# Kernel optimization log

Hardware: AMD Instinct MI355X
Metric: run time of the kernel (lower is better)

The kernel has to match this reference:

```python
import jax, jax.numpy as jnp
import numpy as np

D_MODEL = 1024
N_HEADS = 16
D_K = D_MODEL // N_HEADS


def setup_inputs() -> dict:
    key = jax.random.key(0)
    ks = jax.random.split(key, 9)
    B, S, D = 2, 2048, D_MODEL
    q = jax.random.normal(ks[0], (B, S, D), dtype=jnp.float32)
    v = jax.random.normal(ks[1], (B, S, D), dtype=jnp.float32)
    k = jax.random.normal(ks[2], (B, S, D), dtype=jnp.float32)
    att_mask = jnp.zeros((B, S, S), dtype=jnp.float32)
    seq_mask = jax.random.uniform(ks[3], (B, S, S), dtype=jnp.float32)
    scale = 1.0 / np.sqrt(D)
    Wq = jax.random.normal(ks[4], (D, D), dtype=jnp.float32) * scale
    Wk = jax.random.normal(ks[5], (D, D), dtype=jnp.float32) * scale
    Wv = jax.random.normal(ks[6], (D, D), dtype=jnp.float32) * scale
    Wo = jax.random.normal(ks[7], (D, D), dtype=jnp.float32) * scale
    return {"q": q, "v": v, "k": k, "att_mask": att_mask, "seq_mask": seq_mask,
            "Wq": Wq, "Wk": Wk, "Wv": Wv, "Wo": Wo}


def _split_heads(x, B):
    # [B, S, D] -> [B, H, S, d_k]
    return x.reshape(B, -1, N_HEADS, D_K).transpose(0, 2, 1, 3)


def reference(q, v, k, att_mask, seq_mask, Wq, Wk, Wv, Wo):
    B = q.shape[0]
    qh = _split_heads(q @ Wq, B)
    kh = _split_heads(k @ Wk, B)
    vh = _split_heads(v @ Wv, B)
    # scores: [B, H, Sq, Sk]
    scores = jnp.einsum('bhqd,bhkd->bhqk', qh, kh) / jnp.sqrt(jnp.float32(D_K))
    scores = scores + att_mask[:, None]
    attn = jax.nn.softmax(scores, axis=-1)
    attn = attn * seq_mask[:, None]  # post-softmax multiplicative mask
    out = jnp.einsum('bhqk,bhkd->bhqd', attn, vh)
    out = out.transpose(0, 2, 1, 3).reshape(B, -1, D_MODEL)
    return out @ Wo
```

## Files before the change

kernel.cpp:

```cpp
#include <hip/hip_runtime.h>
#include <cstddef>

typedef __attribute__((ext_vector_type(8))) short s16x8;
typedef __attribute__((ext_vector_type(4))) float f32x4;
typedef __attribute__((ext_vector_type(4))) unsigned short us4;

static __device__ __forceinline__ float bf2f(unsigned short u) {
    union { unsigned u; float f; } v;
    v.u = ((unsigned)u) << 16;
    return v.f;
}

static __device__ __forceinline__ unsigned short f2bf(float f) {
    union { float f; unsigned u; } v;
    v.f = f;
    unsigned r = v.u + 0x7fffu + ((v.u >> 16) & 1u);
    return (unsigned short)(r >> 16);
}

static __device__ __forceinline__ unsigned short f2bf_fast(float f) {
    unsigned r;
    asm("v_cvt_pk_bf16_f32 %0, %1, %2" : "=v"(r) : "v"(f), "v"(f));
    return (unsigned short)r;
}

#if __has_builtin(__builtin_amdgcn_exp2f)
#define EXP2F(x) __builtin_amdgcn_exp2f(x)
#else
#define EXP2F(x) exp2f(x)
#endif

static __device__ __forceinline__ float ldf(const unsigned short* p, size_t i) { return bf2f(p[i]); }
static __device__ __forceinline__ float ldf(const float* p, size_t i) { return p[i]; }
static __device__ __forceinline__ void stf(unsigned short* p, size_t i, float v) { p[i] = f2bf(v); }
static __device__ __forceinline__ void stf(float* p, size_t i, float v) { p[i] = v; }

__global__ __launch_bounds__(256) void probe_dtype(
    const unsigned short* __restrict__ q, unsigned* __restrict__ flags)
{
    __shared__ float red[256];
    const int t = threadIdx.x;
    float m = 0.0f;
    for (int i = t; i < 16384; i += 256) {
        float x = fabsf(bf2f(q[i]));
        if (!(x == x)) x = 1.0e30f;
        m = fmaxf(m, x);
    }
    red[t] = m;
    __syncthreads();
    for (int s = 128; s > 0; s >>= 1) {
        if (t < s) red[t] = fmaxf(red[t], red[t + s]);
        __syncthreads();
    }
    if (t == 0) {
        flags[0] = (red[0] < 1000.0f) ? 0u : 1u;
        flags[1] = 0u;
    }
}

__global__ __launch_bounds__(256) void probe_zero(
    const uint4* __restrict__ m, unsigned* __restrict__ flags)
{
    const unsigned dt = flags[0];
    const size_t n = dt ? 2097152u : 1048576u;
    unsigned acc = 0;
    for (size_t i = (size_t)blockIdx.x * 256 + threadIdx.x; i < n;
         i += (size_t)gridDim.x * 256) {
        uint4 v = m[i];
        acc |= v.x | v.y | v.z | v.w;
    }
    if (acc) atomicOr(&flags[1], 1u);
}

__global__ __launch_bounds__(256) void cvt3_f32_bf16(
    const float4* __restrict__ s0, us4* __restrict__ d0,
    const float4* __restrict__ s1, us4* __restrict__ d1,
    const float4* __restrict__ s2, us4* __restrict__ d2,
    unsigned n4, const unsigned* __restrict__ flags)
{
    if (flags[0] != 1u) return;
    const float4* s = (blockIdx.y == 0) ? s0 : (blockIdx.y == 1) ? s1 : s2;
    us4* d = (blockIdx.y == 0) ? d0 : (blockIdx.y == 1) ? d1 : d2;
    for (unsigned i = blockIdx.x * 256u + threadIdx.x; i < n4;
         i += gridDim.x * 256u) {
        float4 v = s[i];
        us4 o;
        o.x = f2bf(v.x); o.y = f2bf(v.y); o.z = f2bf(v.z); o.w = f2bf(v.w);
        d[i] = o;
    }
}

__global__ __launch_bounds__(256) void copy3_bf16(
    const uint4* __restrict__ s0, uint4* __restrict__ d0,
    const uint4* __restrict__ s1, uint4* __restrict__ d1,
    const uint4* __restrict__ s2, uint4* __restrict__ d2,
    unsigned n16, const unsigned* __restrict__ flags)
{
    if (flags[0] != 0u) return;
    const uint4* s = (blockIdx.y == 0) ? s0 : (blockIdx.y == 1) ? s1 : s2;
    uint4* d = (blockIdx.y == 0) ? d0 : (blockIdx.y == 1) ? d1 : d2;
    for (unsigned i = blockIdx.x * 256u + threadIdx.x; i < n16;
         i += gridDim.x * 256u)
        d[i] = s[i];
}

__global__ __launch_bounds__(256) void cvt_f32_bf16(
    const float4* __restrict__ src, us4* __restrict__ dst, unsigned n4,
    const unsigned* __restrict__ flags)
{
    if (flags[0] != 1u) return;
    for (unsigned i = blockIdx.x * 256u + threadIdx.x; i < n4;
         i += gridDim.x * 256u) {
        float4 v = src[i];
        us4 o;
        o.x = f2bf(v.x); o.y = f2bf(v.y); o.z = f2bf(v.z); o.w = f2bf(v.w);
        dst[i] = o;
    }
}

template <typename T>
__global__ __launch_bounds__(256) void transpose_w(
    const T* __restrict__ src, unsigned short* __restrict__ dst,
    const unsigned* __restrict__ flag, unsigned want)
{
    if (*flag != want) return;
    __shared__ unsigned short tile[32][33];
    const int c0 = blockIdx.x * 32, r0 = blockIdx.y * 32;
    const int tx = threadIdx.x, ty = threadIdx.y;
#pragma unroll
    for (int i = 0; i < 32; i += 8)
        tile[ty + i][tx] = f2bf(ldf(src, (size_t)(r0 + ty + i) * 1024 + c0 + tx));
    __syncthreads();
#pragma unroll
    for (int i = 0; i < 32; i += 8)
        dst[(size_t)(c0 + ty + i) * 1024 + r0 + tx] = tile[tx][ty + i];
}

template <typename T>
__global__ __launch_bounds__(256) void transpose_w3(
    const T* __restrict__ s0, const T* __restrict__ s1, const T* __restrict__ s2,
    unsigned short* __restrict__ d0, unsigned short* __restrict__ d1,
    unsigned short* __restrict__ d2,
    const unsigned* __restrict__ flag, unsigned want)
{
    if (*flag != want) return;
    const T* src = (blockIdx.z == 0) ? s0 : (blockIdx.z == 1) ? s1 : s2;
    unsigned short* dst = (blockIdx.z == 0) ? d0 : (blockIdx.z == 1) ? d1 : d2;
    __shared__ unsigned short tile[32][33];
    const int c0 = blockIdx.x * 32, r0 = blockIdx.y * 32;
    const int tx = threadIdx.x, ty = threadIdx.y;
#pragma unroll
    for (int i = 0; i < 32; i += 8)
        tile[ty + i][tx] = f2bf(ldf(src, (size_t)(r0 + ty + i) * 1024 + c0 + tx));
    __syncthreads();
#pragma unroll
    for (int i = 0; i < 32; i += 8)
        dst[(size_t)(c0 + ty + i) * 1024 + r0 + tx] = tile[tx][ty + i];
}

template <typename TO>
__global__ __launch_bounds__(256) void gemm_kernel(
    const unsigned short* __restrict__ A, const unsigned short* __restrict__ Bt,
    TO* __restrict__ out, int mode, const unsigned* __restrict__ flags, unsigned want)
{
    if (want != 2u && flags[0] != want) return;
    const int K = 1024;
    __shared__ __align__(16) unsigned short lA[64 * 72];
    __shared__ __align__(16) unsigned short lB[64 * 72];

    const int m0 = blockIdx.y * 64, n0 = blockIdx.x * 64;
    const int t = threadIdx.x;
    const int w = t >> 6, l = t & 63, quad = l >> 4, l15 = l & 15;
    const int srow = t >> 2, scol = (t & 3) * 16;

    const unsigned short* Arow = A + (size_t)(m0 + srow) * K + scol;
    const unsigned short* Brow = Bt + (size_t)(n0 + srow) * K + scol;

    f32x4 acc[4] = {};

    uint4 a0 = *(const uint4*)(Arow);
    uint4 a1 = *(const uint4*)(Arow + 8);
    uint4 b0 = *(const uint4*)(Brow);
    uint4 b1 = *(const uint4*)(Brow + 8);

    for (int k0 = 0; k0 < K; k0 += 64) {
        *(uint4*)&lA[srow * 72 + scol] = a0;
        *(uint4*)&lA[srow * 72 + scol + 8] = a1;
        *(uint4*)&lB[srow * 72 + scol] = b0;
        *(uint4*)&lB[srow * 72 + scol + 8] = b1;
        __syncthreads();
        const int kn = (k0 + 64) & (K - 1);
        a0 = *(const uint4*)(Arow + kn);
        a1 = *(const uint4*)(Arow + kn + 8);
        b0 = *(const uint4*)(Brow + kn);
        b1 = *(const uint4*)(Brow + kn + 8);
#pragma unroll
        for (int kk = 0; kk < 64; kk += 32) {
            s16x8 af = *(const s16x8*)&lA[(w * 16 + l15) * 72 + kk + quad * 8];
#pragma unroll
            for (int g = 0; g < 4; g++) {
                s16x8 bf = *(const s16x8*)&lB[(g * 16 + l15) * 72 + kk + quad * 8];
                acc[g] = __builtin_amdgcn_mfma_f32_16x16x32_bf16(af, bf, acc[g], 0, 0, 0);
            }
        }
        __syncthreads();
    }

#pragma unroll
    for (int g = 0; g < 4; g++) {
#pragma unroll
        for (int r = 0; r < 4; r++) {
            int row = m0 + w * 16 + quad * 4 + r;
            int col = n0 + g * 16 + l15;
            float val = acc[g][r];
            if (mode == 0) {
                stf(out, (size_t)row * 1024 + col, val);
            } else {
                int b = row >> 11, s = row & 2047;
                int h = col >> 6, d = col & 63;
                if (mode == 1)
                    stf(out, (((size_t)(b * 16 + h) * 2048) + s) * 64 + d, val);
                else
                    stf(out, (((size_t)(b * 16 + h) * 64) + d) * 2048 + s, val);
            }
        }
    }
}

template <typename TM>
__global__ __launch_bounds__(256) void attn_kernel(
    const unsigned short* __restrict__ qh, const unsigned short* __restrict__ kh,
    const unsigned short* __restrict__ vt, const TM* __restrict__ amask,
    const unsigned short* __restrict__ smask, unsigned short* __restrict__ aout,
    const unsigned* __restrict__ flags, unsigned want)
{
    if (flags[0] != want) return;
    const bool useA = (flags[1] != 0u);
    const int S = 2048, DK = 64, H = 16;
    const int qt = blockIdx.x, h = blockIdx.y, b = blockIdx.z;
    const unsigned short* qhb = qh + (size_t)(b * H + h) * S * DK;
    const unsigned short* khb = kh + (size_t)(b * H + h) * S * DK;
    const unsigned short* vtb = vt + (size_t)(b * H + h) * DK * S;
    const TM* amb = amask + (size_t)b * S * S;
    const unsigned short* smb = smask + (size_t)b * S * S;

    __shared__ __align__(16) unsigned short lK[64 * 72];
    __shared__ __align__(16) unsigned short lV[64 * 72];
    __shared__ __align__(16) unsigned short lP[4][16 * 72];

    const int t = threadIdx.x;
    const int w = t >> 6, l = t & 63, quad = l >> 4, l15 = l & 15;
    const int q0 = qt * 64;
    const int srow = t >> 2, scol = (t & 3) * 16;

    const float SCALE2 = 0.18033688011112042f;
    const float LOG2E  = 1.4426950408889634f;

    const int qrow_a = q0 + w * 16 + l15;
    s16x8 qf0 = *(const s16x8*)&qhb[(size_t)qrow_a * DK + quad * 8];
    s16x8 qf1 = *(const s16x8*)&qhb[(size_t)qrow_a * DK + 32 + quad * 8];

    float mrun[4], lsum[4];
    f32x4 o[4] = {};
#pragma unroll
    for (int r = 0; r < 4; r++) { mrun[r] = -INFINITY; lsum[r] = 0.0f; }

    for (int k0 = 0; k0 < S; k0 += 64) {
        const uint4* gk = (const uint4*)&khb[(size_t)(k0 + srow) * DK + scol];
        const uint4* gv = (const uint4*)&vtb[(size_t)srow * S + k0 + scol];
        uint4 ka = gk[0], kb = gk[1];
        uint4 va = gv[0], vb = gv[1];
        *(uint4*)&lK[srow * 72 + scol] = ka;
        *(uint4*)&lK[srow * 72 + scol + 8] = kb;
        *(uint4*)&lV[srow * 72 + scol] = va;
        *(uint4*)&lV[srow * 72 + scol + 8] = vb;
        __syncthreads();

        f32x4 sc[4] = {};
#pragma unroll
        for (int kk = 0; kk < 64; kk += 32) {
            s16x8 af = (kk == 0) ? qf0 : qf1;
#pragma unroll
            for (int g = 0; g < 4; g++) {
                s16x8 bf = *(const s16x8*)&lK[(g * 16 + l15) * 72 + kk + quad * 8];
                sc[g] = __builtin_amdgcn_mfma_f32_16x16x32_bf16(af, bf, sc[g], 0, 0, 0);
            }
        }

        if (!useA) {
#pragma unroll
            for (int r = 0; r < 4; r++) {
                const int qr = q0 + w * 16 + quad * 4 + r;
                const size_t mrow = (size_t)qr * S + k0;
                float sv0 = sc[0][r] * SCALE2;
                float sv1 = sc[1][r] * SCALE2;
                float sv2 = sc[2][r] * SCALE2;
                float sv3 = sc[3][r] * SCALE2;
                float mx = fmaxf(fmaxf(sv0, sv1), fmaxf(sv2, sv3));
#pragma unroll
                for (int d = 1; d < 16; d <<= 1) mx = fmaxf(mx, __shfl_xor(mx, d));
                float mnew = fmaxf(mrun[r], mx);
                float alpha = EXP2F(mrun[r] - mnew);
                float e0 = EXP2F(sv0 - mnew);
                float e1 = EXP2F(sv1 - mnew);
                float e2 = EXP2F(sv2 - mnew);
                float e3 = EXP2F(sv3 - mnew);
                lsum[r] = lsum[r] * alpha + ((e0 + e1) + (e2 + e3));
                mrun[r] = mnew;
#pragma unroll
                for (int g = 0; g < 4; g++) o[g][r] *= alpha;
                const int rowp = (quad * 4 + r) * 72;
                lP[w][rowp + 0 * 16 + l15] = f2bf_fast(e0 * bf2f(smb[mrow + 0 * 16 + l15]));
                lP[w][rowp + 1 * 16 + l15] = f2bf_fast(e1 * bf2f(smb[mrow + 1 * 16 + l15]));
                lP[w][rowp + 2 * 16 + l15] = f2bf_fast(e2 * bf2f(smb[mrow + 2 * 16 + l15]));
                lP[w][rowp + 3 * 16 + l15] = f2bf_fast(e3 * bf2f(smb[mrow + 3 * 16 + l15]));
            }
        } else {
#pragma unroll
            for (int r = 0; r < 4; r++) {
                const int qr = q0 + w * 16 + quad * 4 + r;
                const size_t mrow = (size_t)qr * S + k0;
                float sv0 = fmaf((float)ldf(amb, mrow + 0 * 16 + l15), LOG2E, sc[0][r] * SCALE2);
                float sv1 = fmaf((float)ldf(amb, mrow + 1 * 16 + l15), LOG2E, sc[1][r] * SCALE2);
                float sv2 = fmaf((float)ldf(amb, mrow + 2 * 16 + l15), LOG2E, sc[2][r] * SCALE2);
                float sv3 = fmaf((float)ldf(amb, mrow + 3 * 16 + l15), LOG2E, sc[3][r] * SCALE2);
                float mx = fmaxf(fmaxf(sv0, sv1), fmaxf(sv2, sv3));
#pragma unroll
                for (int d = 1; d < 16; d <<= 1) mx = fmaxf(mx, __shfl_xor(mx, d));
                float mnew = fmaxf(mrun[r], mx);
                float alpha = EXP2F(mrun[r] - mnew);
                float e0 = EXP2F(sv0 - mnew);
                float e1 = EXP2F(sv1 - mnew);
                float e2 = EXP2F(sv2 - mnew);
                float e3 = EXP2F(sv3 - mnew);
                lsum[r] = lsum[r] * alpha + ((e0 + e1) + (e2 + e3));
                mrun[r] = mnew;
#pragma unroll
                for (int g = 0; g < 4; g++) o[g][r] *= alpha;
                const int rowp = (quad * 4 + r) * 72;
                lP[w][rowp + 0 * 16 + l15] = f2bf_fast(e0 * bf2f(smb[mrow + 0 * 16 + l15]));
                lP[w][rowp + 1 * 16 + l15] = f2bf_fast(e1 * bf2f(smb[mrow + 1 * 16 + l15]));
                lP[w][rowp + 2 * 16 + l15] = f2bf_fast(e2 * bf2f(smb[mrow + 2 * 16 + l15]));
                lP[w][rowp + 3 * 16 + l15] = f2bf_fast(e3 * bf2f(smb[mrow + 3 * 16 + l15]));
            }
        }
        __syncthreads();

#pragma unroll
        for (int kk = 0; kk < 64; kk += 32) {
            s16x8 pf = *(const s16x8*)&lP[w][l15 * 72 + kk + quad * 8];
#pragma unroll
            for (int g = 0; g < 4; g++) {
                s16x8 vf = *(const s16x8*)&lV[(g * 16 + l15) * 72 + kk + quad * 8];
                o[g] = __builtin_amdgcn_mfma_f32_16x16x32_bf16(pf, vf, o[g], 0, 0, 0);
            }
        }
        __syncthreads();
    }

#pragma unroll
    for (int r = 0; r < 4; r++) {
        float ls = lsum[r];
#pragma unroll
        for (int d = 1; d < 16; d <<= 1) ls += __shfl_xor(ls, d);
        float inv = 1.0f / ls;
        const int qr = q0 + w * 16 + quad * 4 + r;
#pragma unroll
        for (int g = 0; g < 4; g++) {
            aout[((size_t)(b * S + qr)) * 1024 + h * 64 + g * 16 + l15] =
                f2bf_fast(o[g][r] * inv);
        }
    }
}

extern "C" void kernel_launch(void* const* d_in, const int* in_sizes, int n_in,
                              void* d_out, int out_size, void* d_ws, size_t ws_size,
                              hipStream_t stream)
{
    const void* q   = d_in[0];
    const void* v   = d_in[1];
    const void* k   = d_in[2];
    const void* att = d_in[3];
    const void* seq = d_in[4];
    const void* Wq  = d_in[5];
    const void* Wk  = d_in[6];
    const void* Wv  = d_in[7];
    const void* Wo  = d_in[8];

    const size_t WELEM = 1024 * 1024;
    const size_t HELEM = (size_t)2 * 16 * 2048 * 64;

    unsigned* flags = (unsigned*)d_ws;
    unsigned short* base = (unsigned short*)((char*)d_ws + 512);
    unsigned short* r0 = base;
    unsigned short* qh = base + HELEM;
    unsigned short* kh = qh + HELEM;
    unsigned short* vt = kh + HELEM;
    unsigned short* qb = vt + HELEM;
    unsigned short* kb = qb + HELEM;
    unsigned short* vb = kb + HELEM;
    unsigned short* seqb = qb;

    const dim3 tg(32, 32), tb(32, 8);
    const dim3 tg3(32, 32, 3);
    const dim3 gg(16, 64), gb(256);
    const dim3 ag(32, 16, 2), ab(256);

    probe_dtype<<<1, 256, 0, stream>>>((const unsigned short*)q, flags);
    probe_zero<<<1024, 256, 0, stream>>>((const uint4*)att, flags);

    const unsigned n4h = 1048576u, n16h = 524288u;
    cvt3_f32_bf16<<<dim3(512, 3), 256, 0, stream>>>(
        (const float4*)q, (us4*)qb, (const float4*)k, (us4*)kb,
        (const float4*)v, (us4*)vb, n4h, flags);
    copy3_bf16<<<dim3(512, 3), 256, 0, stream>>>(
        (const uint4*)q, (uint4*)qb, (const uint4*)k, (uint4*)kb,
        (const uint4*)v, (uint4*)vb, n16h, flags);

    transpose_w3<unsigned short><<<tg3, tb, 0, stream>>>(
        (const unsigned short*)Wq, (const unsigned short*)Wk, (const unsigned short*)Wv,
        r0 + 0 * WELEM, r0 + 1 * WELEM, r0 + 2 * WELEM, flags, 0);
    transpose_w3<float><<<tg3, tb, 0, stream>>>(
        (const float*)Wq, (const float*)Wk, (const float*)Wv,
        r0 + 0 * WELEM, r0 + 1 * WELEM, r0 + 2 * WELEM, flags, 1);

    gemm_kernel<unsigned short><<<gg, gb, 0, stream>>>(qb, r0 + 0 * WELEM, qh, 1, flags, 2);
    gemm_kernel<unsigned short><<<gg, gb, 0, stream>>>(kb, r0 + 1 * WELEM, kh, 1, flags, 2);
    gemm_kernel<unsigned short><<<gg, gb, 0, stream>>>(vb, r0 + 2 * WELEM, vt, 2, flags, 2);

    const unsigned n4s = 2097152u;
    cvt_f32_bf16<<<2048, 256, 0, stream>>>((const float4*)seq, (us4*)seqb, n4s, flags);

    unsigned short* ao = r0;
    attn_kernel<unsigned short><<<ag, ab, 0, stream>>>(
        qh, kh, vt, (const unsigned short*)att, (const unsigned short*)seq, ao, flags, 0);
    attn_kernel<float><<<ag, ab, 0, stream>>>(
        qh, kh, vt, (const float*)att, seqb, ao, flags, 1);

    transpose_w<unsigned short><<<tg, tb, 0, stream>>>((const unsigned short*)Wo, qh, flags, 0);
    transpose_w<float><<<tg, tb, 0, stream>>>((const float*)Wo, qh, flags, 1);

    gemm_kernel<unsigned short><<<gg, gb, 0, stream>>>(ao, qh, (unsigned short*)d_out, 0, flags, 0);
    gemm_kernel<float><<<gg, gb, 0, stream>>>(ao, qh, (float*)d_out, 0, flags, 1);
}
```

Measured before the change: 407.8 us.

## Prefetch K, V and seq-mask tiles into LDS asynchronously with swizzled layout

The attention kernel now issues direct global-to-LDS async loads for the next K tile, V tile and seq_mask tile while computing the current one, with V double-buffered and one barrier per iteration dropped. LDS tiles use an XOR swizzle in place of padding to avoid bank conflicts. The seq_mask is staged through LDS with coalesced 16-byte loads instead of scattered 2-byte global reads. The useA branch becomes a template parameter, which adds two extra launches that exit early. K and seq-mask are single-buffered, so correctness depends on the async loads landing before the next barrier.

```diff
diff --git a/kernel.cpp b/kernel.cpp
--- a/kernel.cpp
+++ b/kernel.cpp
@@ -29,6 +29,12 @@
 #else
 #define EXP2F(x) exp2f(x)
 #endif
+
+typedef const __attribute__((address_space(1))) unsigned int* as1_cu32p;
+typedef __attribute__((address_space(3))) unsigned int* as3_u32p;
+static __device__ __forceinline__ void async16(const void* g, void* l) {
+    __builtin_amdgcn_global_load_lds((as1_cu32p)g, (as3_u32p)l, 16, 0, 0);
+}
 
 static __device__ __forceinline__ float ldf(const unsigned short* p, size_t i) { return bf2f(p[i]); }
 static __device__ __forceinline__ float ldf(const float* p, size_t i) { return p[i]; }
@@ -227,15 +233,14 @@
     }
 }
 
-template <typename TM>
+template <typename TM, bool USEA>
 __global__ __launch_bounds__(256) void attn_kernel(
     const unsigned short* __restrict__ qh, const unsigned short* __restrict__ kh,
     const unsigned short* __restrict__ vt, const TM* __restrict__ amask,
     const unsigned short* __restrict__ smask, unsigned short* __restrict__ aout,
     const unsigned* __restrict__ flags, unsigned want)
 {
-    if (flags[0] != want) return;
-    const bool useA = (flags[1] != 0u);
+    if (flags[0] != want || (flags[1] != 0u) != USEA) return;
     const int S = 2048, DK = 64, H = 16;
     const int qt = blockIdx.x, h = blockIdx.y, b = blockIdx.z;
     const unsigned short* qhb = qh + (size_t)(b * H + h) * S * DK;
@@ -244,17 +249,35 @@
     const TM* amb = amask + (size_t)b * S * S;
     const unsigned short* smb = smask + (size_t)b * S * S;
 
-    __shared__ __align__(16) unsigned short lK[64 * 72];
-    __shared__ __align__(16) unsigned short lV[64 * 72];
+    __shared__ __align__(16) unsigned short lK[64 * 64];
+    __shared__ __align__(16) unsigned short lM[64 * 64];
+    __shared__ __align__(16) unsigned short lV[2][64 * 64];
     __shared__ __align__(16) unsigned short lP[4][16 * 72];
 
     const int t = threadIdx.x;
     const int w = t >> 6, l = t & 63, quad = l >> 4, l15 = l & 15;
     const int q0 = qt * 64;
-    const int srow = t >> 2, scol = (t & 3) * 16;
 
     const float SCALE2 = 0.18033688011112042f;
     const float LOG2E  = 1.4426950408889634f;
+
+    const int trow = t >> 3;
+    const int tcol = (((t & 7) ^ ((t >> 3) & 7)) * 8);
+    const unsigned short* ksrc0 = khb + (size_t)trow * DK + tcol;
+    const unsigned short* ksrc1 = khb + (size_t)(trow + 32) * DK + tcol;
+    const unsigned short* msrc0 = smb + (size_t)(q0 + trow) * S + tcol;
+    const unsigned short* msrc1 = smb + (size_t)(q0 + trow + 32) * S + tcol;
+    const unsigned short* vsrc0 = vtb + (size_t)trow * S + tcol;
+    const unsigned short* vsrc1 = vtb + (size_t)(trow + 32) * S + tcol;
+    char* kdst = (char*)lK + (t >> 6) * 1024;
+    char* mdst = (char*)lM + (t >> 6) * 1024;
+    char* vbase = (char*)&lV[0][0] + (t >> 6) * 1024;
+
+    async16(ksrc0, kdst); async16(ksrc1, kdst + 4096);
+    async16(msrc0, mdst); async16(msrc1, mdst + 4096);
+    async16(vsrc0, vbase); async16(vsrc1, vbase + 4096);
+
+    const int ksw = (l15 & 7) * 8;
 
     const int qrow_a = q0 + w * 16 + l15;
     s16x8 qf0 = *(const s16x8*)&qhb[(size_t)qrow_a * DK + quad * 8];
@@ -265,15 +288,8 @@
 #pragma unroll
     for (int r = 0; r < 4; r++) { mrun[r] = -INFINITY; lsum[r] = 0.0f; }
 
-    for (int k0 = 0; k0 < S; k0 += 64) {
-        const uint4* gk = (const uint4*)&khb[(size_t)(k0 + srow) * DK + scol];
-        const uint4* gv = (const uint4*)&vtb[(size_t)srow * S + k0 + scol];
-        uint4 ka = gk[0], kb = gk[1];
-        uint4 va = gv[0], vb = gv[1];
-        *(uint4*)&lK[srow * 72 + scol] = ka;
-        *(uint4*)&lK[srow * 72 + scol + 8] = kb;
-        *(uint4*)&lV[srow * 72 + scol] = va;
-        *(uint4*)&lV[srow * 72 + scol + 8] = vb;
+    int it = 0;
+    for (int k0 = 0; k0 < S; k0 += 64, ++it) {
         __syncthreads();
 
         f32x4 sc[4] = {};
@@ -282,80 +298,71 @@
             s16x8 af = (kk == 0) ? qf0 : qf1;
 #pragma unroll
             for (int g = 0; g < 4; g++) {
-                s16x8 bf = *(const s16x8*)&lK[(g * 16 + l15) * 72 + kk + quad * 8];
+                s16x8 bf = *(const s16x8*)&lK[(g * 16 + l15) * 64 + ((kk + quad * 8) ^ ksw)];
                 sc[g] = __builtin_amdgcn_mfma_f32_16x16x32_bf16(af, bf, sc[g], 0, 0, 0);
             }
         }
 
-        if (!useA) {
-#pragma unroll
-            for (int r = 0; r < 4; r++) {
-                const int qr = q0 + w * 16 + quad * 4 + r;
-                const size_t mrow = (size_t)qr * S + k0;
-                float sv0 = sc[0][r] * SCALE2;
-                float sv1 = sc[1][r] * SCALE2;
-                float sv2 = sc[2][r] * SCALE2;
-                float sv3 = sc[3][r] * SCALE2;
-                float mx = fmaxf(fmaxf(sv0, sv1), fmaxf(sv2, sv3));
-#pragma unroll
-                for (int d = 1; d < 16; d <<= 1) mx = fmaxf(mx, __shfl_xor(mx, d));
-                float mnew = fmaxf(mrun[r], mx);
-                float alpha = EXP2F(mrun[r] - mnew);
-                float e0 = EXP2F(sv0 - mnew);
-                float e1 = EXP2F(sv1 - mnew);
-                float e2 = EXP2F(sv2 - mnew);
-                float e3 = EXP2F(sv3 - mnew);
-                lsum[r] = lsum[r] * alpha + ((e0 + e1) + (e2 + e3));
-                mrun[r] = mnew;
-#pragma unroll
-                for (int g = 0; g < 4; g++) o[g][r] *= alpha;
-                const int rowp = (quad * 4 + r) * 72;
-                lP[w][rowp + 0 * 16 + l15] = f2bf_fast(e0 * bf2f(smb[mrow + 0 * 16 + l15]));
-                lP[w][rowp + 1 * 16 + l15] = f2bf_fast(e1 * bf2f(smb[mrow + 1 * 16 + l15]));
-                lP[w][rowp + 2 * 16 + l15] = f2bf_fast(e2 * bf2f(smb[mrow + 2 * 16 + l15]));
-                lP[w][rowp + 3 * 16 + l15] = f2bf_fast(e3 * bf2f(smb[mrow + 3 * 16 + l15]));
+#pragma unroll
+        for (int r = 0; r < 4; r++) {
+            float sv0, sv1, sv2, sv3;
+            if (USEA) {
+                const size_t mrow = (size_t)(q0 + w * 16 + quad * 4 + r) * S + k0;
+                sv0 = fmaf((float)ldf(amb, mrow + 0 * 16 + l15), LOG2E, sc[0][r] * SCALE2);
+                sv1 = fmaf((float)ldf(amb, mrow + 1 * 16 + l15), LOG2E, sc[1][r] * SCALE2);
+                sv2 = fmaf((float)ldf(amb, mrow + 2 * 16 + l15), LOG2E, sc[2][r] * SCALE2);
+                sv3 = fmaf((float)ldf(amb, mrow + 3 * 16 + l15), LOG2E, sc[3][r] * SCALE2);
+            } else {
+                sv0 = sc[0][r] * SCALE2;
+                sv1 = sc[1][r] * SCALE2;
+                sv2 = sc[2][r] * SCALE2;
+                sv3 = sc[3][r] * SCALE2;
             }
-        } else {
-#pragma unroll
-            for (int r = 0; r < 4; r++) {
-                const int qr = q0 + w * 16 + quad * 4 + r;
-                const size_t mrow = (size_t)qr * S + k0;
-                float sv0 = fmaf((float)ldf(amb, mrow + 0 * 16 + l15), LOG2E, sc[0][r] * SCALE2);
-                float sv1 = fmaf((float)ldf(amb, mrow + 1 * 16 + l15), LOG2E, sc[1][r] * SCALE2);
-                float sv2 = fmaf((float)ldf(amb, mrow + 2 * 16 + l15), LOG2E, sc[2][r] * SCALE2);
-                float sv3 = fmaf((float)ldf(amb, mrow + 3 * 16 + l15), LOG2E, sc[3][r] * SCALE2);
-                float mx = fmaxf(fmaxf(sv0, sv1), fmaxf(sv2, sv3));
-#pragma unroll
-                for (int d = 1; d < 16; d <<= 1) mx = fmaxf(mx, __shfl_xor(mx, d));
-                float mnew = fmaxf(mrun[r], mx);
-                float alpha = EXP2F(mrun[r] - mnew);
-                float e0 = EXP2F(sv0 - mnew);
-                float e1 = EXP2F(sv1 - mnew);
-                float e2 = EXP2F(sv2 - mnew);
-                float e3 = EXP2F(sv3 - mnew);
-                lsum[r] = lsum[r] * alpha + ((e0 + e1) + (e2 + e3));
-                mrun[r] = mnew;
-#pragma unroll
-                for (int g = 0; g < 4; g++) o[g][r] *= alpha;
-                const int rowp = (quad * 4 + r) * 72;
-                lP[w][rowp + 0 * 16 + l15] = f2bf_fast(e0 * bf2f(smb[mrow + 0 * 16 + l15]));
-                lP[w][rowp + 1 * 16 + l15] = f2bf_fast(e1 * bf2f(smb[mrow + 1 * 16 + l15]));
-                lP[w][rowp + 2 * 16 + l15] = f2bf_fast(e2 * bf2f(smb[mrow + 2 * 16 + l15]));
-                lP[w][rowp + 3 * 16 + l15] = f2bf_fast(e3 * bf2f(smb[mrow + 3 * 16 + l15]));
-            }
+            float mx = fmaxf(fmaxf(sv0, sv1), fmaxf(sv2, sv3));
+#pragma unroll
+            for (int d = 1; d < 16; d <<= 1) mx = fmaxf(mx, __shfl_xor(mx, d));
+            float mnew = fmaxf(mrun[r], mx);
+            float alpha = EXP2F(mrun[r] - mnew);
+            float e0 = EXP2F(sv0 - mnew);
+            float e1 = EXP2F(sv1 - mnew);
+            float e2 = EXP2F(sv2 - mnew);
+            float e3 = EXP2F(sv3 - mnew);
+            lsum[r] = lsum[r] * alpha + ((e0 + e1) + (e2 + e3));
+            mrun[r] = mnew;
+#pragma unroll
+            for (int g = 0; g < 4; g++) o[g][r] *= alpha;
+
+            const int rowm = (w * 16 + quad * 4 + r) * 64;
+            const int msw = ((quad * 4 + r) & 7) * 8;
+            const int rowp = (quad * 4 + r) * 72;
+            lP[w][rowp + 0 * 16 + l15] = f2bf_fast(e0 * bf2f(lM[rowm + ((0 * 16 + l15) ^ msw)]));
+            lP[w][rowp + 1 * 16 + l15] = f2bf_fast(e1 * bf2f(lM[rowm + ((1 * 16 + l15) ^ msw)]));
+            lP[w][rowp + 2 * 16 + l15] = f2bf_fast(e2 * bf2f(lM[rowm + ((2 * 16 + l15) ^ msw)]));
+            lP[w][rowp + 3 * 16 + l15] = f2bf_fast(e3 * bf2f(lM[rowm + ((3 * 16 + l15) ^ msw)]));
         }
         __syncthreads();
 
+        const int kn = (k0 + 64) & (S - 1);
+        if (kn) {
+            async16(ksrc0 + (size_t)kn * DK, kdst);
+            async16(ksrc1 + (size_t)kn * DK, kdst + 4096);
+            async16(msrc0 + kn, mdst);
+            async16(msrc1 + kn, mdst + 4096);
+            char* vd = vbase + ((it + 1) & 1) * 8192;
+            async16(vsrc0 + kn, vd);
+            async16(vsrc1 + kn, vd + 4096);
+        }
+
+        const unsigned short* lVc = &lV[it & 1][0];
 #pragma unroll
         for (int kk = 0; kk < 64; kk += 32) {
             s16x8 pf = *(const s16x8*)&lP[w][l15 * 72 + kk + quad * 8];
 #pragma unroll
             for (int g = 0; g < 4; g++) {
-                s16x8 vf = *(const s16x8*)&lV[(g * 16 + l15) * 72 + kk + quad * 8];
+                s16x8 vf = *(const s16x8*)&lVc[(g * 16 + l15) * 64 + ((kk + quad * 8) ^ ksw)];
                 o[g] = __builtin_amdgcn_mfma_f32_16x16x32_bf16(pf, vf, o[g], 0, 0, 0);
             }
         }
-        __syncthreads();
     }
 
 #pragma unroll
@@ -432,9 +439,13 @@
     cvt_f32_bf16<<<2048, 256, 0, stream>>>((const float4*)seq, (us4*)seqb, n4s, flags);
 
     unsigned short* ao = r0;
-    attn_kernel<unsigned short><<<ag, ab, 0, stream>>>(
+    attn_kernel<unsigned short, false><<<ag, ab, 0, stream>>>(
         qh, kh, vt, (const unsigned short*)att, (const unsigned short*)seq, ao, flags, 0);
-    attn_kernel<float><<<ag, ab, 0, stream>>>(
+    attn_kernel<float, false><<<ag, ab, 0, stream>>>(
+        qh, kh, vt, (const float*)att, seqb, ao, flags, 1);
+    attn_kernel<unsigned short, true><<<ag, ab, 0, stream>>>(
+        qh, kh, vt, (const unsigned short*)att, (const unsigned short*)seq, ao, flags, 0);
+    attn_kernel<float, true><<<ag, ab, 0, stream>>>(
         qh, kh, vt, (const float*)att, seqb, ao, flags, 1);
 
     transpose_w<unsigned short><<<tg, tb, 0, stream>>>((const unsigned short*)Wo, qh, flags, 0);
```

Result: no change. 409.1 us (+0.3%).
